# Optimization experiments

Measured on AMD Instinct MI355X. Metric: run time of the kernel, lower is better.

The kernel has to match this reference:

```python
import jax, jax.numpy as jnp
import numpy as np

LEAK = 0.2
NUM_GRAPHS = 64


def _gat(h_in, src, dst, eh, W, att_src, att_dst, att_edge, lin_edge_W, bias, N):
    # PyG GATConv with edge_dim, concat=False (mean over heads)
    H, C = att_src.shape
    h = (h_in @ W).reshape(N, H, C)                      # [N,H,C]
    e = (eh @ lin_edge_W).reshape(-1, H, C)              # [Eaug,H,C]
    a_s = jnp.einsum('nhc,hc->nh', h, att_src)           # [N,H]
    a_d = jnp.einsum('nhc,hc->nh', h, att_dst)
    a_e = jnp.einsum('ehc,hc->eh', e, att_edge)          # [Eaug,H]
    score = jax.nn.leaky_relu(a_s[src] + a_d[dst] + a_e, LEAK)
    # scatter-softmax over incoming edges of each destination node
    m = jax.ops.segment_max(score, dst, num_segments=N)
    ex = jnp.exp(score - m[dst])
    den = jax.ops.segment_sum(ex, dst, num_segments=N)
    alpha = ex / den[dst]                                # [Eaug,H]
    out = jax.ops.segment_sum(alpha[:, :, None] * h[src], dst, num_segments=N)
    return out.mean(axis=1) + bias                       # concat=False -> head mean


def setup_inputs() -> dict:
    key = jax.random.key(0)
    ks = jax.random.split(key, 32)
    N, E, F, FE, HID, H, NT = 30000, 480000, 64, 16, 64, 4, 16
    Cin1 = F + HID
    s = 0.05
    d = {
        'x': jax.random.normal(ks[0], (N, F), jnp.float32),
        'edge_attr': jax.random.normal(ks[1], (E, FE), jnp.float32),
        'node_emb': jax.random.normal(ks[2], (NT, HID), jnp.float32) * s,
        'edge_W': jax.random.normal(ks[3], (FE, HID), jnp.float32) * s,
        'edge_b': jnp.zeros((HID,), jnp.float32),
        'W1': jax.random.normal(ks[4], (Cin1, H * HID), jnp.float32) * s,
        'as1': jax.random.normal(ks[5], (H, HID), jnp.float32) * s,
        'ad1': jax.random.normal(ks[6], (H, HID), jnp.float32) * s,
        'ae1': jax.random.normal(ks[7], (H, HID), jnp.float32) * s,
        'leW1': jax.random.normal(ks[8], (HID, H * HID), jnp.float32) * s,
        'b1': jnp.zeros((HID,), jnp.float32),
        'W2': jax.random.normal(ks[9], (HID, H * HID), jnp.float32) * s,
        'as2': jax.random.normal(ks[10], (H, HID), jnp.float32) * s,
        'ad2': jax.random.normal(ks[11], (H, HID), jnp.float32) * s,
        'ae2': jax.random.normal(ks[12], (H, HID), jnp.float32) * s,
        'leW2': jax.random.normal(ks[13], (HID, H * HID), jnp.float32) * s,
        'b2': jnp.zeros((HID,), jnp.float32),
        'sage_Wl': jax.random.normal(ks[14], (HID, HID), jnp.float32) * s,
        'sage_bl': jnp.zeros((HID,), jnp.float32),
        'sage_Wr': jax.random.normal(ks[15], (HID, HID), jnp.float32) * s,
        'lin1_W': jax.random.normal(ks[16], (HID, HID), jnp.float32) * s,
        'lin1_b': jnp.zeros((HID,), jnp.float32),
        'lin2_W': jax.random.normal(ks[17], (HID, HID), jnp.float32) * s,
        'lin2_b': jnp.zeros((HID,), jnp.float32),
        'tel_W': jax.random.normal(ks[18], (HID, 1), jnp.float32) * s,
        'tel_b': jnp.zeros((1,), jnp.float32),
        'comp_W': jax.random.normal(ks[19], (HID, 1), jnp.float32) * s,
        'comp_b': jnp.zeros((1,), jnp.float32),
        'pch_W': jax.random.normal(ks[20], (HID, 1), jnp.float32) * s,
        'pch_b': jnp.zeros((1,), jnp.float32),
        'edge_index': jax.random.randint(ks[21], (2, E), 0, N, jnp.int32),
        'batch': jnp.sort(jax.random.randint(ks[22], (N,), 0, NUM_GRAPHS, jnp.int32)),
        'node_type': jax.random.randint(ks[23], (N,), 0, NT, jnp.int32),
    }
    return d


def reference(x, edge_attr, node_emb, edge_W, edge_b,
              W1, as1, ad1, ae1, leW1, b1,
              W2, as2, ad2, ae2, leW2, b2,
              sage_Wl, sage_bl, sage_Wr,
              lin1_W, lin1_b, lin2_W, lin2_b,
              tel_W, tel_b, comp_W, comp_b, pch_W, pch_b,
              edge_index, batch, node_type):
    N = x.shape[0]
    src0, dst0 = edge_index[0], edge_index[1]

    h0 = jnp.concatenate([x, node_emb[node_type]], axis=-1)   # [N, F+HID]
    eh = edge_attr @ edge_W + edge_b                          # [E, HID]

    # GATConv default add_self_loops=True, fill_value='mean' on edge_attr
    loop = jnp.arange(N, dtype=src0.dtype)
    src = jnp.concatenate([src0, loop])
    dst = jnp.concatenate([dst0, loop])
    eh_aug = jnp.concatenate([eh, jnp.broadcast_to(eh.mean(axis=0), (N, eh.shape[1]))], axis=0)

    h1 = jax.nn.elu(_gat(h0, src, dst, eh_aug, W1, as1, ad1, ae1, leW1, b1, N))
    h2 = jax.nn.elu(_gat(h1, src, dst, eh_aug, W2, as2, ad2, ae2, leW2, b2, N))

    # SAGEConv: mean neighbor aggregation (src->dst) + root transform
    deg = jax.ops.segment_sum(jnp.ones_like(dst0, dtype=h2.dtype), dst0, num_segments=N)
    agg = jax.ops.segment_sum(h2[src0], dst0, num_segments=N) / jnp.clip(deg, 1.0)[:, None]
    h3 = jax.nn.elu(agg @ sage_Wl + sage_bl + h2 @ sage_Wr)

    # global mean pool per graph
    cnt = jax.ops.segment_sum(jnp.ones((N,), h3.dtype), batch, num_segments=NUM_GRAPHS)
    g = jax.ops.segment_sum(h3, batch, num_segments=NUM_GRAPHS) / jnp.clip(cnt, 1.0)[:, None]

    g = jax.nn.elu(g @ lin1_W + lin1_b)                       # dropout inactive (eval)
    g = g @ lin2_W + lin2_b
    return (g @ tel_W + tel_b, g @ comp_W + comp_b, g @ pch_W + pch_b)
```

## Files before the change

### kernel.cpp

```cpp
#include <hip/hip_runtime.h>
#include <hip/hip_fp16.h>
#include <math.h>

#define NN 30000
#define NE 480000
#define FEA 16
#define HID 64
#define NG 64
#define LEAKK 0.2f

#define S_AEL1   0
#define S_AEL2   4
#define S_KF1    16
#define S_C1     80
#define S_KF2    88
#define S_C2     152
#define S_MS1    160
#define S_MD1    672
#define S_MS2    1184
#define S_MD2    1440
#define S_EAS    1700

#define BT1H 0
#define BT1L 20480
#define BT2H 40960
#define BT2L 57344
#define BT3H 73728
#define BT3L 81920

typedef __attribute__((ext_vector_type(8))) short short8;
typedef __attribute__((ext_vector_type(4))) float f32x4;

__device__ __forceinline__ float eluf(float v) { return v > 0.f ? v : expm1f(v); }
__device__ __forceinline__ float leakyf(float v) { return v >= 0.f ? v : LEAKK * v; }
__device__ __forceinline__ void fma4(float4& a, float w, const float4& x) {
    a.x += w * x.x; a.y += w * x.y; a.z += w * x.z; a.w += w * x.w;
}
__device__ __forceinline__ unsigned bf16pack(float a, float b) {
    unsigned ua = __float_as_uint(a), ub = __float_as_uint(b);
    ua = (ua + 0x7FFFu + ((ua >> 16) & 1u)) >> 16;
    ub = (ub + 0x7FFFu + ((ub >> 16) & 1u)) >> 16;
    return ua | (ub << 16);
}
__device__ __forceinline__ unsigned short bf1(float v) {
    unsigned u = __float_as_uint(v);
    return (unsigned short)((u + 0x7FFFu + ((u >> 16) & 1u)) >> 16);
}
__device__ __forceinline__ float bf1tof(unsigned short h) {
    return __uint_as_float(((unsigned)h) << 16);
}
__device__ __forceinline__ uint2 bfpack4(float a, float b, float c, float d) {
    return make_uint2(bf16pack(a, b), bf16pack(c, d));
}
__device__ __forceinline__ float4 bf16x4(uint2 p) {
    float4 r;
    r.x = __uint_as_float(p.x << 16);
    r.y = __uint_as_float(p.x & 0xFFFF0000u);
    r.z = __uint_as_float(p.y << 16);
    r.w = __uint_as_float(p.y & 0xFFFF0000u);
    return r;
}
__device__ __forceinline__ unsigned h2pack(float a, float b) {
    __half2 h = __floats2half2_rn(a, b);
    return *(unsigned*)&h;
}
__device__ __forceinline__ float2 h2unpack(unsigned u) {
    __half2 h = *(__half2*)&u;
    return __half22float2(h);
}
__device__ __forceinline__ float4 h4tof(uint2 p) {
    float2 lo = h2unpack(p.x), hi = h2unpack(p.y);
    return make_float4(lo.x, lo.y, hi.x, hi.y);
}
__device__ __forceinline__ float4 escore4(float4 a, float4 b, float4 c) {
    float4 r;
    r.x = expf(leakyf(a.x + b.x + c.x));
    r.y = expf(leakyf(a.y + b.y + c.y));
    r.z = expf(leakyf(a.z + b.z + c.z));
    r.w = expf(leakyf(a.w + b.w + c.w));
    return r;
}


__global__ __launch_bounds__(256) void cm_prepw_kernel(
    const int* __restrict__ dst, const float* __restrict__ EA,
    int* __restrict__ cnt, int* __restrict__ rank,
    const float* __restrict__ W1, const float* __restrict__ W2,
    const float* __restrict__ Wl, const float* __restrict__ Wr,
    const float* __restrict__ emb,
    const float* __restrict__ leW1, const float* __restrict__ aew1,
    const float* __restrict__ leW2, const float* __restrict__ aew2,
    const float* __restrict__ edge_W, const float* __restrict__ edge_b,
    const float* __restrict__ as1, const float* __restrict__ ad1,
    const float* __restrict__ as2, const float* __restrict__ ad2,
    const int* __restrict__ batch,
    unsigned short* __restrict__ BT,
    float* __restrict__ S, int* __restrict__ goff) {
    int t = threadIdx.x, bx = blockIdx.x;
    if (bx < 176) {
        int i = bx * 256 + t;
        float v = 0.f;
        int dsti = -1;
        if (i < 16384) {
            int kk = i >> 6, c = i & 63;
            int h = kk >> 6, k = kk & 63;
            v = 0.25f * W1[k * 256 + h * 64 + c];
            dsti = BT1H + c * 320 + kk;
        } else if (i < 20480) {
            int j2 = i - 16384;
            int r2 = j2 >> 6, c = j2 & 63;
            int tau = r2 >> 2, h = r2 & 3;
            float acc = 0.f;
            for (int j = 0; j < 64; j++)
                acc += emb[tau * 64 + j] * W1[(64 + j) * 256 + h * 64 + c];
            v = 0.25f * acc;
            dsti = BT1H + c * 320 + 256 + r2;
        } else if (i < 36864) {
            int j = i - 20480;
            int kk = j >> 6, c = j & 63;
            int h = kk >> 6, k = kk & 63;
            v = 0.25f * W2[k * 256 + h * 64 + c];
            dsti = BT2H + c * 256 + kk;
        } else if (i < 45056) {
            int j = i - 36864;
            int k = j >> 6, c = j & 63;
            v = (k < 64) ? Wl[k * 64 + c] : Wr[(k - 64) * 64 + c];
            dsti = BT3H + c * 128 + k;
        }
        if (dsti >= 0) {
            unsigned short hi = bf1(v);
            unsigned short lo = bf1(v - bf1tof(hi));
            BT[dsti] = hi;
            BT[dsti + 20480 - ((dsti >= BT2H) ? ((dsti >= BT3H) ? 12288 : 4096) : 0)] = lo;
        }
        return;
    }
    if (bx < 178) {
        int i = (bx - 176) * 256 + t;
        int k = i >> 2, h = i & 3;
        float s = 0.f, d = 0.f;
        for (int c = 0; c < 64; c++) {
            float w = W1[k * 256 + h * 64 + c];
            s += w * as1[h * 64 + c];
            d += w * ad1[h * 64 + c];
        }
        S[S_MS1 + i] = s; S[S_MD1 + i] = d;
        return;
    }
    if (bx == 178) {
        int k = t >> 2, h = t & 3;
        float s = 0.f, d = 0.f;
        for (int c = 0; c < 64; c++) {
            float w = W2[k * 256 + h * 64 + c];
            s += w * as2[h * 64 + c];
            d += w * ad2[h * 64 + c];
        }
        S[S_MS2 + t] = s; S[S_MD2 + t] = d;
        return;
    }
    if (bx == 179) {
        __shared__ float M1s[256], M2s[256];
        {
            int k = t >> 2, h = t & 3;
            float m1 = 0.f, m2 = 0.f;
            for (int c = 0; c < 64; c++) {
                m1 += leW1[k * 256 + h * 64 + c] * aew1[h * 64 + c];
                m2 += leW2[k * 256 + h * 64 + c] * aew2[h * 64 + c];
            }
            M1s[t] = m1; M2s[t] = m2;
        }
        __syncthreads();
        if (t < 64) {
            int f = t >> 2, h = t & 3;
            float k1 = 0.f, k2 = 0.f;
            for (int k = 0; k < 64; k++) {
                k1 += edge_W[f * 64 + k] * M1s[k * 4 + h];
                k2 += edge_W[f * 64 + k] * M2s[k * 4 + h];
            }
            S[S_KF1 + t] = k1; S[S_KF2 + t] = k2;
        } else if (t < 68) {
            int h = t - 64;
            float c1 = 0.f, c2 = 0.f;
            for (int k = 0; k < 64; k++) {
                c1 += edge_b[k] * M1s[k * 4 + h];
                c2 += edge_b[k] * M2s[k * 4 + h];
            }
            S[S_C1 + h] = c1; S[S_C2 + h] = c2;
        }
        return;
    }
    if (bx == 180) {
        if (t > NG) return;
        int lo = 0, hi = NN;
        while (lo < hi) {
            int mid = (lo + hi) >> 1;
            if (batch[mid] < t) lo = mid + 1; else hi = mid;
        }
        goff[t] = lo;
        return;
    }
    if (bx < 245) {
        __shared__ float4 red4[16];
        int cb = bx - 181;
        int c4 = (t & 3) * 4;
        int r0 = cb * 64 + (t >> 2);
        float4 a0 = {0, 0, 0, 0}, a1 = a0, a2 = a0, a3 = a0;
        for (int r = r0; r < NE; r += 16384) {
            int r1 = r + 4096, r2 = r + 8192, r3 = r + 12288;
            float4 v0 = *(const float4*)(EA + (size_t)r * FEA + c4);
            float4 v1 = (r1 < NE) ? *(const float4*)(EA + (size_t)r1 * FEA + c4)
                                  : make_float4(0, 0, 0, 0);
            float4 v2 = (r2 < NE) ? *(const float4*)(EA + (size_t)r2 * FEA + c4)
                                  : make_float4(0, 0, 0, 0);
            float4 v3 = (r3 < NE) ? *(const float4*)(EA + (size_t)r3 * FEA + c4)
                                  : make_float4(0, 0, 0, 0);
            a0.x += v0.x; a0.y += v0.y; a0.z += v0.z; a0.w += v0.w;
            a1.x += v1.x; a1.y += v1.y; a1.z += v1.z; a1.w += v1.w;
            a2.x += v2.x; a2.y += v2.y; a2.z += v2.z; a2.w += v2.w;
            a3.x += v3.x; a3.y += v3.y; a3.z += v3.z; a3.w += v3.w;
        }
        float4 acc;
        acc.x = (a0.x + a1.x) + (a2.x + a3.x);
        acc.y = (a0.y + a1.y) + (a2.y + a3.y);
        acc.z = (a0.z + a1.z) + (a2.z + a3.z);
        acc.w = (a0.w + a1.w) + (a2.w + a3.w);
#pragma unroll
        for (int mask = 4; mask < 64; mask <<= 1) {
            acc.x += __shfl_xor(acc.x, mask, 64);
            acc.y += __shfl_xor(acc.y, mask, 64);
            acc.z += __shfl_xor(acc.z, mask, 64);
            acc.w += __shfl_xor(acc.w, mask, 64);
        }
        int lane = t & 63, wid = t >> 6;
        if (lane < 4) red4[wid * 4 + lane] = acc;
        __syncthreads();
        if (t < 4) {
            float4 a = red4[t], b = red4[4 + t], c = red4[8 + t], d = red4[12 + t];
            atomicAdd(&S[S_EAS + t * 4 + 0], a.x + b.x + c.x + d.x);
            atomicAdd(&S[S_EAS + t * 4 + 1], a.y + b.y + c.y + d.y);
            atomicAdd(&S[S_EAS + t * 4 + 2], a.z + b.z + c.z + d.z);
            atomicAdd(&S[S_EAS + t * 4 + 3], a.w + b.w + c.w + d.w);
        }
        return;
    }
    int base = (bx - 245) * 1024;
    int e0 = base + t, e1 = e0 + 256, e2 = e0 + 512, e3 = e0 + 768;
    int d0 = (e0 < NE) ? dst[e0] : 0;
    int d1 = (e1 < NE) ? dst[e1] : 0;
    int d2 = (e2 < NE) ? dst[e2] : 0;
    int d3 = (e3 < NE) ? dst[e3] : 0;
    int r0 = 0, r1 = 0, r2 = 0, r3 = 0;
    if (e0 < NE) r0 = atomicAdd(&cnt[d0 * 8], 1);
    if (e1 < NE) r1 = atomicAdd(&cnt[d1 * 8], 1);
    if (e2 < NE) r2 = atomicAdd(&cnt[d2 * 8], 1);
    if (e3 < NE) r3 = atomicAdd(&cnt[d3 * 8], 1);
    if (e0 < NE) rank[e0] = r0;
    if (e1 < NE) rank[e1] = r1;
    if (e2 < NE) rank[e2] = r2;
    if (e3 < NE) rank[e3] = r3;
}

__global__ void scan_blocks_kernel(const int* __restrict__ cnt, int* __restrict__ eoff,
                                   int* __restrict__ bsum) {
    __shared__ int wsum[16];
    int t = threadIdx.x;
    int i = blockIdx.x * 1024 + t;
    int v = (i < NN) ? cnt[i * 8] : 0;
    int lane = t & 63;
    int incl = v;
#pragma unroll
    for (int ofs = 1; ofs < 64; ofs <<= 1) {
        int u = __shfl_up(incl, ofs, 64);
        if (lane >= ofs) incl += u;
    }
    int wid = t >> 6;
    if (lane == 63) wsum[wid] = incl;
    __syncthreads();
    if (t < 16) {
        int s = wsum[t];
#pragma unroll
        for (int ofs = 1; ofs < 16; ofs <<= 1) {
            int u = __shfl_up(s, ofs, 64);
            if (t >= ofs) s += u;
        }
        wsum[t] = s;
    }
    __syncthreads();
    int excl = incl - v + (wid > 0 ? wsum[wid - 1] : 0);
    if (i < NN) eoff[i] = excl;
    if (t == 1023) bsum[blockIdx.x] = excl + v;
}

__global__ __launch_bounds__(256) void scanadd_attn_kernel(
    const int* __restrict__ bsum, int* __restrict__ eoff,
    const float* __restrict__ x, const float* __restrict__ node_emb,
    const int* __restrict__ node_type, float* __restrict__ S,
    float* __restrict__ as_, float* __restrict__ ad_, unsigned* __restrict__ xb) {
    __shared__ float xt[64 * 132];
    __shared__ float ms[512], md[512];
    __shared__ int ntS[64];
    int t = threadIdx.x;
    if (blockIdx.x < 118) {
        int j = blockIdx.x >> 2;
        int pref = 0;
        for (int u = 0; u < j; u++) pref += bsum[u];
        int i = blockIdx.x * 256 + t;
        if (i < NN) eoff[i] += pref;
        if (i == 0) eoff[NN] = NE;
        return;
    }
    if (blockIdx.x == 118) {
        if (t < 8) {
            int h = t & 3;
            const float* KF = (t < 4) ? (S + S_KF1) : (S + S_KF2);
            const float* C  = (t < 4) ? (S + S_C1)  : (S + S_C2);
            float acc = (float)NE * C[h];
            for (int f = 0; f < 16; f++) acc += S[S_EAS + f] * KF[f * 4 + h];
            S[((t < 4) ? S_AEL1 : S_AEL2) + h] = acc;
        }
        return;
    }
    int n0 = (blockIdx.x - 119) * 64;
    if (t < 64) {
        int n = n0 + t;
        ntS[t] = (n < NN) ? node_type[n] : 0;
    }
    for (int i = t; i < 512; i += 256) { ms[i] = S[S_MS1 + i]; md[i] = S[S_MD1 + i]; }
    __syncthreads();
    for (int i = t; i < 1024; i += 256) {
        int r = i >> 4, c4 = (i & 15) * 4;
        int n = n0 + r;
        float4 f = {0, 0, 0, 0};
        if (n < NN) f = *(const float4*)(x + (size_t)n * 64 + c4);
        *(float4*)&xt[r * 132 + c4] = f;
    }
    for (int i = t; i < 1024; i += 256) {
        int r = i >> 4, c4 = (i & 15) * 4;
        int n = n0 + r;
        float4 f = {0, 0, 0, 0};
        if (n < NN) f = *(const float4*)(node_emb + (size_t)ntS[r] * 64 + c4);
        *(float4*)&xt[r * 132 + 64 + c4] = f;
    }
    __syncthreads();
    for (int i = t; i < 2048; i += 256) {
        int r = i >> 5, u = i & 31;
        int n = n0 + r;
        if (n < NN)
            xb[(size_t)n * 32 + u] = bf16pack(xt[r * 132 + 2 * u], xt[r * 132 + 2 * u + 1]);
    }
    int r = t >> 2, h = t & 3;
    float s = 0.f, d = 0.f;
#pragma unroll 8
    for (int k = 0; k < 128; k++) {
        float xv = xt[r * 132 + k];
        s += xv * ms[k * 4 + h];
        d += xv * md[k * 4 + h];
    }
    int n = n0 + r;
    if (n < NN) { as_[n * 4 + h] = s; ad_[n * 4 + h] = d; }
}

__global__ __launch_bounds__(256) void scatter_proj_kernel(
    const int* __restrict__ src, const int* __restrict__ dst,
    const float* __restrict__ EA, const float* __restrict__ S,
    const float* __restrict__ as_, const float* __restrict__ ad_,
    const int* __restrict__ node_type,
    const int* __restrict__ eoff, const int* __restrict__ rank,
    uint4* __restrict__ recs) {
    __shared__ float KF1s[64], KF2s[64], Cs[8];
    int t = threadIdx.x;
    if (t < 64) { KF1s[t] = S[S_KF1 + t]; KF2s[t] = S[S_KF2 + t]; }
    else if (t < 72) { int q = t - 64; Cs[q] = (q < 4) ? S[S_C1 + q] : S[S_C2 + q - 4]; }
    __syncthreads();
    int e0 = blockIdx.x * 512 + t;
#pragma unroll
    for (int u = 0; u < 2; u++) {
        int e = e0 + u * 256;
        if (e < NE) {
            int s = src[e], d = dst[e];
            float a1[4], a2[4];
#pragma unroll
            for (int h = 0; h < 4; h++) { a1[h] = Cs[h]; a2[h] = Cs[4 + h]; }
            const float4* EA4 = (const float4*)(EA + (size_t)e * FEA);
#pragma unroll
            for (int q = 0; q < 4; q++) {
                float4 v = EA4[q];
                float vv[4] = {v.x, v.y, v.z, v.w};
#pragma unroll
                for (int j = 0; j < 4; j++) {
                    int f = q * 4 + j;
#pragma unroll
                    for (int h = 0; h < 4; h++) {
                        a1[h] += vv[j] * KF1s[f * 4 + h];
                        a2[h] += vv[j] * KF2s[f * 4 + h];
                    }
                }
            }
            int pos = eoff[d] + rank[e];
            float4 asv = ((const float4*)as_)[s];
            float4 adv = ((const float4*)ad_)[d];
            float4 w1 = escore4(asv, adv, make_float4(a1[0], a1[1], a1[2], a1[3]));
            uint4 lo = make_uint4(h2pack(w1.x, w1.y), h2pack(w1.z, w1.w),
                                  h2pack(a2[0], a2[1]), h2pack(a2[2], a2[3]));
            uint4 hi = make_uint4((unsigned)(s | (node_type[s] << 16)), (unsigned)d, 0u, 0u);
            recs[2 * pos] = lo;
            recs[2 * pos + 1] = hi;
        }
    }
}

__global__ __launch_bounds__(256) void score2_kernel(
    uint4* __restrict__ recs,
    const float* __restrict__ as_, const float* __restrict__ ad_,
    int* __restrict__ sepc) {
    int p = blockIdx.x * 256 + threadIdx.x;
    uint2 a2h = ((const uint2*)recs)[4 * p + 1];
    int2 sd = ((const int2*)recs)[4 * p + 2];
    int s = sd.x & 0xFFFF;
    float4 w2 = escore4(((const float4*)as_)[s], ((const float4*)ad_)[sd.y], h4tof(a2h));
    ((uint2*)recs)[4 * p + 1] = make_uint2(h2pack(w2.x, w2.y), h2pack(w2.z, w2.w));
    sepc[p] = sd.x;
}

__global__ __launch_bounds__(256) void agg_gat1_kernel(
    const int* __restrict__ eoff, const uint4* __restrict__ recs,
    const unsigned* __restrict__ xb,
    const int* __restrict__ node_type,
    const float* __restrict__ as_, const float* __restrict__ ad_,
    const float* __restrict__ S, uint2* __restrict__ aggb) {
    int n = blockIdx.x * 4 + (threadIdx.x >> 6);
    if (n >= NN) return;
    int lane = threadIdx.x & 63;
    int sub = lane >> 4, ch = lane & 15;
    const uint2* Xb = (const uint2*)xb;
    const int* RI = (const int*)recs;
    const uint2* RW = (const uint2*)recs;
    float4 asn = ((const float4*)as_)[n];
    float4 adn = ((const float4*)ad_)[n];
    float4 a0 = {0, 0, 0, 0}, a1 = a0, a2 = a0, a3 = a0, dn = a0, tw = a0;
    int b = eoff[n], e_end = eoff[n + 1];
    int nE = e_end - b;
    int i = sub;
    for (; i + 4 < nE; i += 8) {
        int p0 = b + i, p1 = p0 + 4;
        int q0 = RI[8 * p0 + 4], q1 = RI[8 * p1 + 4];
        int s0 = q0 & 0xFFFF, t0 = q0 >> 16;
        int s1 = q1 & 0xFFFF, t1 = q1 >> 16;
        float4 w0 = h4tof(RW[4 * p0]), w1 = h4tof(RW[4 * p1]);
        float4 x0 = bf16x4(Xb[(size_t)s0 * 16 + ch]);
        float4 x1 = bf16x4(Xb[(size_t)s1 * 16 + ch]);
        fma4(a0, w0.x, x0); fma4(a1, w0.y, x0); fma4(a2, w0.z, x0); fma4(a3, w0.w, x0);
        fma4(a0, w1.x, x1); fma4(a1, w1.y, x1); fma4(a2, w1.z, x1); fma4(a3, w1.w, x1);
        dn.x += w0.x + w1.x; dn.y += w0.y + w1.y;
        dn.z += w0.z + w1.z; dn.w += w0.w + w1.w;
        if (ch == t0) { tw.x += w0.x; tw.y += w0.y; tw.z += w0.z; tw.w += w0.w; }
        if (ch == t1) { tw.x += w1.x; tw.y += w1.y; tw.z += w1.z; tw.w += w1.w; }
    }
    for (; i < nE; i += 4) {
        int p0 = b + i;
        int q0 = RI[8 * p0 + 4];
        int s0 = q0 & 0xFFFF, t0 = q0 >> 16;
        float4 w0 = h4tof(RW[4 * p0]);
        float4 x0 = bf16x4(Xb[(size_t)s0 * 16 + ch]);
        fma4(a0, w0.x, x0); fma4(a1, w0.y, x0); fma4(a2, w0.z, x0); fma4(a3, w0.w, x0);
        dn.x += w0.x; dn.y += w0.y; dn.z += w0.z; dn.w += w0.w;
        if (ch == t0) { tw.x += w0.x; tw.y += w0.y; tw.z += w0.z; tw.w += w0.w; }
    }
    if (sub == 0) {
        const float inv = 1.f / (float)NE;
        float e0 = expf(leakyf(asn.x + adn.x + S[S_AEL1 + 0] * inv));
        float e1 = expf(leakyf(asn.y + adn.y + S[S_AEL1 + 1] * inv));
        float e2 = expf(leakyf(asn.z + adn.z + S[S_AEL1 + 2] * inv));
        float e3 = expf(leakyf(asn.w + adn.w + S[S_AEL1 + 3] * inv));
        float4 xs = bf16x4(Xb[(size_t)n * 16 + ch]);
        fma4(a0, e0, xs); fma4(a1, e1, xs); fma4(a2, e2, xs); fma4(a3, e3, xs);
        dn.x += e0; dn.y += e1; dn.z += e2; dn.w += e3;
        int tn = node_type[n];
        if (ch == tn) { tw.x += e0; tw.y += e1; tw.z += e2; tw.w += e3; }
    }
#pragma unroll
    for (int mask = 16; mask < 64; mask <<= 1) {
        a0.x += __shfl_xor(a0.x, mask, 64); a0.y += __shfl_xor(a0.y, mask, 64);
        a0.z += __shfl_xor(a0.z, mask, 64); a0.w += __shfl_xor(a0.w, mask, 64);
        a1.x += __shfl_xor(a1.x, mask, 64); a1.y += __shfl_xor(a1.y, mask, 64);
        a1.z += __shfl_xor(a1.z, mask, 64); a1.w += __shfl_xor(a1.w, mask, 64);
        a2.x += __shfl_xor(a2.x, mask, 64); a2.y += __shfl_xor(a2.y, mask, 64);
        a2.z += __shfl_xor(a2.z, mask, 64); a2.w += __shfl_xor(a2.w, mask, 64);
        a3.x += __shfl_xor(a3.x, mask, 64); a3.y += __shfl_xor(a3.y, mask, 64);
        a3.z += __shfl_xor(a3.z, mask, 64); a3.w += __shfl_xor(a3.w, mask, 64);
        dn.x += __shfl_xor(dn.x, mask, 64); dn.y += __shfl_xor(dn.y, mask, 64);
        dn.z += __shfl_xor(dn.z, mask, 64); dn.w += __shfl_xor(dn.w, mask, 64);
        tw.x += __shfl_xor(tw.x, mask, 64); tw.y += __shfl_xor(tw.y, mask, 64);
        tw.z += __shfl_xor(tw.z, mask, 64); tw.w += __shfl_xor(tw.w, mask, 64);
    }
    if (sub == 0) {
        float i0 = 1.f / dn.x, i1 = 1.f / dn.y, i2 = 1.f / dn.z, i3 = 1.f / dn.w;
        uint2* A2 = aggb + (size_t)n * 80;
        A2[ch]      = bfpack4(a0.x * i0, a0.y * i0, a0.z * i0, a0.w * i0);
        A2[16 + ch] = bfpack4(a1.x * i1, a1.y * i1, a1.z * i1, a1.w * i1);
        A2[32 + ch] = bfpack4(a2.x * i2, a2.y * i2, a2.z * i2, a2.w * i2);
        A2[48 + ch] = bfpack4(a3.x * i3, a3.y * i3, a3.z * i3, a3.w * i3);
        A2[64 + ch] = bfpack4(tw.x * i0, tw.y * i1, tw.z * i2, tw.w * i3);
    }
}

__global__ __launch_bounds__(256) void agg_gat2_kernel(
    const int* __restrict__ eoff, const uint4* __restrict__ recs,
    const unsigned* __restrict__ h1b,
    const float* __restrict__ as_, const float* __restrict__ ad_,
    const float* __restrict__ S, uint2* __restrict__ aggb) {
    int n = blockIdx.x * 4 + (threadIdx.x >> 6);
    if (n >= NN) return;
    int lane = threadIdx.x & 63;
    int sub = lane >> 4, ch = lane & 15;
    const uint2* Xb = (const uint2*)h1b;
    const int* RI = (const int*)recs;
    const uint2* RW = (const uint2*)recs;
    float4 asn = ((const float4*)as_)[n];
    float4 adn = ((const float4*)ad_)[n];
    float4 a0 = {0, 0, 0, 0}, a1 = a0, a2 = a0, a3 = a0, dn = a0;
    int b = eoff[n], e = eoff[n + 1];
    int nE = e - b;
    int i = sub;
    for (; i + 4 < nE; i += 8) {
        int p0 = b + i, p1 = p0 + 4;
        int s0 = RI[8 * p0 + 4] & 0xFFFF, s1 = RI[8 * p1 + 4] & 0xFFFF;
        float4 w0 = h4tof(RW[4 * p0 + 1]), w1 = h4tof(RW[4 * p1 + 1]);
        float4 x0 = bf16x4(Xb[(size_t)s0 * 16 + ch]);
        float4 x1 = bf16x4(Xb[(size_t)s1 * 16 + ch]);
        fma4(a0, w0.x, x0); fma4(a1, w0.y, x0); fma4(a2, w0.z, x0); fma4(a3, w0.w, x0);
        fma4(a0, w1.x, x1); fma4(a1, w1.y, x1); fma4(a2, w1.z, x1); fma4(a3, w1.w, x1);
        dn.x += w0.x + w1.x; dn.y += w0.y + w1.y;
        dn.z += w0.z + w1.z; dn.w += w0.w + w1.w;
    }
    for (; i < nE; i += 4) {
        int p0 = b + i;
        int s0 = RI[8 * p0 + 4] & 0xFFFF;
        float4 w0 = h4tof(RW[4 * p0 + 1]);
        float4 x0 = bf16x4(Xb[(size_t)s0 * 16 + ch]);
        fma4(a0, w0.x, x0); fma4(a1, w0.y, x0); fma4(a2, w0.z, x0); fma4(a3, w0.w, x0);
        dn.x += w0.x; dn.y += w0.y; dn.z += w0.z; dn.w += w0.w;
    }
    if (sub == 0) {
        const float inv = 1.f / (float)NE;
        float e0 = expf(leakyf(asn.x + adn.x + S[S_AEL2 + 0] * inv));
        float e1 = expf(leakyf(asn.y + adn.y + S[S_AEL2 + 1] * inv));
        float e2 = expf(leakyf(asn.z + adn.z + S[S_AEL2 + 2] * inv));
        float e3 = expf(leakyf(asn.w + adn.w + S[S_AEL2 + 3] * inv));
        float4 xs = bf16x4(Xb[(size_t)n * 16 + ch]);
        fma4(a0, e0, xs); fma4(a1, e1, xs); fma4(a2, e2, xs); fma4(a3, e3, xs);
        dn.x += e0; dn.y += e1; dn.z += e2; dn.w += e3;
    }
#pragma unroll
    for (int mask = 16; mask < 64; mask <<= 1) {
        a0.x += __shfl_xor(a0.x, mask, 64); a0.y += __shfl_xor(a0.y, mask, 64);
        a0.z += __shfl_xor(a0.z, mask, 64); a0.w += __shfl_xor(a0.w, mask, 64);
        a1.x += __shfl_xor(a1.x, mask, 64); a1.y += __shfl_xor(a1.y, mask, 64);
        a1.z += __shfl_xor(a1.z, mask, 64); a1.w += __shfl_xor(a1.w, mask, 64);
        a2.x += __shfl_xor(a2.x, mask, 64); a2.y += __shfl_xor(a2.y, mask, 64);
        a2.z += __shfl_xor(a2.z, mask, 64); a2.w += __shfl_xor(a2.w, mask, 64);
        a3.x += __shfl_xor(a3.x, mask, 64); a3.y += __shfl_xor(a3.y, mask, 64);
        a3.z += __shfl_xor(a3.z, mask, 64); a3.w += __shfl_xor(a3.w, mask, 64);
        dn.x += __shfl_xor(dn.x, mask, 64); dn.y += __shfl_xor(dn.y, mask, 64);
        dn.z += __shfl_xor(dn.z, mask, 64); dn.w += __shfl_xor(dn.w, mask, 64);
    }
    if (sub == 0) {
        float i0 = 1.f / dn.x, i1 = 1.f / dn.y, i2 = 1.f / dn.z, i3 = 1.f / dn.w;
        uint2* A2 = aggb + (size_t)n * 64;
        A2[ch]      = bfpack4(a0.x * i0, a0.y * i0, a0.z * i0, a0.w * i0);
        A2[16 + ch] = bfpack4(a1.x * i1, a1.y * i1, a1.z * i1, a1.w * i1);
        A2[32 + ch] = bfpack4(a2.x * i2, a2.y * i2, a2.z * i2, a2.w * i2);
        A2[48 + ch] = bfpack4(a3.x * i3, a3.y * i3, a3.z * i3, a3.w * i3);
    }
}

template <int K, bool DOATT>
__global__ __launch_bounds__(256) void gemm_mfma_kernel(
    const unsigned* __restrict__ A, const unsigned short* __restrict__ bth,
    const unsigned short* __restrict__ btl,
    const float* __restrict__ bias, float* __restrict__ out,
    unsigned short* __restrict__ out16,
    const float* __restrict__ ms_g, const float* __restrict__ md_g,
    float* __restrict__ as_, float* __restrict__ ad_) {
    int t = threadIdx.x;
    int w = t >> 6, l = t & 63;
    int lr = l & 15, lg = l >> 4;
    int m0 = blockIdx.x * 64 + w * 16;
    int am = m0 + lr;
    bool av = am < NN;
    const short8* Arow = (const short8*)A + (size_t)am * (K / 8);
    short8 zz = {0, 0, 0, 0, 0, 0, 0, 0};
    f32x4 acc[4];
#pragma unroll
    for (int ct = 0; ct < 4; ct++) acc[ct] = (f32x4){0.f, 0.f, 0.f, 0.f};
#pragma unroll
    for (int k0 = 0; k0 < K; k0 += 32) {
        short8 a = av ? Arow[(k0 >> 3) + lg] : zz;
#pragma unroll
        for (int ct = 0; ct < 4; ct++) {
            int bo = (ct * 16 + lr) * K + k0 + lg * 8;
            short8 bh = *(const short8*)(bth + bo);
            short8 bl = *(const short8*)(btl + bo);
            acc[ct] = __builtin_amdgcn_mfma_f32_16x16x32_bf16(a, bh, acc[ct], 0, 0, 0);
            acc[ct] = __builtin_amdgcn_mfma_f32_16x16x32_bf16(a, bl, acc[ct], 0, 0, 0);
        }
    }
    f32x4 ps[4], pd[4];
    if (DOATT) {
#pragma unroll
        for (int r = 0; r < 4; r++) {
            ps[r] = (f32x4){0.f, 0.f, 0.f, 0.f};
            pd[r] = (f32x4){0.f, 0.f, 0.f, 0.f};
        }
    }
#pragma unroll
    for (int ct = 0; ct < 4; ct++) {
        int col = ct * 16 + lr;
        float bv = bias[col];
        f32x4 ms4, md4;
        if (DOATT) {
            ms4 = ((const f32x4*)ms_g)[col];
            md4 = ((const f32x4*)md_g)[col];
        }
#pragma unroll
        for (int r = 0; r < 4; r++) {
            int m = m0 + lg * 4 + r;
            float o = eluf(acc[ct][r] + bv);
            if (m < NN) {
                if (out) out[(size_t)m * 64 + col] = o;
                if (out16) out16[(size_t)m * 64 + col] = bf1(o);
            }
            if (DOATT) { ps[r] += o * ms4; pd[r] += o * md4; }
        }
    }
    if (DOATT) {
#pragma unroll
        for (int mk = 1; mk < 16; mk <<= 1)
#pragma unroll
            for (int r = 0; r < 4; r++) {
                ps[r][0] += __shfl_xor(ps[r][0], mk, 64);
                ps[r][1] += __shfl_xor(ps[r][1], mk, 64);
                ps[r][2] += __shfl_xor(ps[r][2], mk, 64);
                ps[r][3] += __shfl_xor(ps[r][3], mk, 64);
                pd[r][0] += __shfl_xor(pd[r][0], mk, 64);
                pd[r][1] += __shfl_xor(pd[r][1], mk, 64);
                pd[r][2] += __shfl_xor(pd[r][2], mk, 64);
                pd[r][3] += __shfl_xor(pd[r][3], mk, 64);
            }
        if (lr == 0) {
#pragma unroll
            for (int r = 0; r < 4; r++) {
                int m = m0 + lg * 4 + r;
                if (m < NN) {
                    *(f32x4*)(as_ + (size_t)m * 4) = ps[r];
                    *(f32x4*)(ad_ + (size_t)m * 4) = pd[r];
                }
            }
        }
    }
}

__global__ __launch_bounds__(256) void sage_agg3_kernel(
    const unsigned* __restrict__ h2b,
    const int* __restrict__ eoff, const int* __restrict__ sepc,
    uint2* __restrict__ AB) {
    int n = blockIdx.x * 16 + (threadIdx.x >> 4);
    if (n >= NN) return;
    int l = threadIdx.x & 15;
    const uint2* Hb = (const uint2*)h2b;
    float ax = 0.f, ay = 0.f, az = 0.f, aw = 0.f;
    int b = eoff[n], e_end = eoff[n + 1];
    int idx = b;
    int stop = b + ((e_end - b) & ~7);
    if (idx < stop) {
        int sreg[8];
#pragma unroll
        for (int u = 0; u < 8; u++) sreg[u] = sepc[idx + u] & 0xFFFF;
        idx += 8;
        while (true) {
            int sn[8];
            bool more = idx < stop;
            if (more) {
#pragma unroll
                for (int u = 0; u < 8; u++) sn[u] = sepc[idx + u] & 0xFFFF;
            }
#pragma unroll
            for (int u = 0; u < 8; u++) {
                float4 v = bf16x4(Hb[(size_t)sreg[u] * 16 + l]);
                ax += v.x; ay += v.y; az += v.z; aw += v.w;
            }
            if (!more) break;
#pragma unroll
            for (int u = 0; u < 8; u++) sreg[u] = sn[u];
            idx += 8;
        }
    }
    for (; idx < e_end; idx++) {
        float4 v0 = bf16x4(Hb[(size_t)(sepc[idx] & 0xFFFF) * 16 + l]);
        ax += v0.x; ay += v0.y; az += v0.z; aw += v0.w;
    }
    float dg = (float)(e_end - b);
    if (dg < 1.f) dg = 1.f;
    float inv = 1.f / dg;
    AB[(size_t)n * 32 + l] = bfpack4(ax * inv, ay * inv, az * inv, aw * inv);
    AB[(size_t)n * 32 + 16 + l] = Hb[(size_t)n * 16 + l];
}

__global__ __launch_bounds__(256) void pool_mlp_kernel(
    const float* __restrict__ h3, const int* __restrict__ goff,
    const float* __restrict__ lin1W, const float* __restrict__ lin1b,
    const float* __restrict__ lin2W, const float* __restrict__ lin2b,
    const float* __restrict__ telW, const float* __restrict__ telb,
    const float* __restrict__ compW, const float* __restrict__ compb,
    const float* __restrict__ pchW, const float* __restrict__ pchb,
    float* __restrict__ out) {
    __shared__ float red[256];
    __shared__ float g[64], G1[64], G2[64];
    int gi = blockIdx.x, t = threadIdx.x;
    int c = t & 63, li = t >> 6;
    int b = goff[gi], e = goff[gi + 1];
    float sum = 0.f;
    for (int r = b + li; r < e; r += 4) sum += h3[(size_t)r * HID + c];
    red[t] = sum;
    __syncthreads();
    if (t < 64) {
        float v = red[t] + red[t + 64] + red[t + 128] + red[t + 192];
        float cntf = (float)(e - b);
        if (cntf < 1.f) cntf = 1.f;
        g[t] = v / cntf;
    }
    __syncthreads();
    {
        float part = 0.f;
#pragma unroll
        for (int k = li * 16; k < li * 16 + 16; k++) part += g[k] * lin1W[k * 64 + c];
        red[t] = part;
        __syncthreads();
        if (t < 64)
            G1[c] = eluf(red[c] + red[c + 64] + red[c + 128] + red[c + 192] + lin1b[c]);
        __syncthreads();
    }
    {
        float part = 0.f;
#pragma unroll
        for (int k = li * 16; k < li * 16 + 16; k++) part += G1[k] * lin2W[k * 64 + c];
        red[t] = part;
        __syncthreads();
        if (t < 64)
            G2[c] = red[c] + red[c + 64] + red[c + 128] + red[c + 192] + lin2b[c];
        __syncthreads();
    }
    if (t < 192) {
        int h = t >> 6, k = t & 63;
        const float* W = (h == 0) ? telW : ((h == 1) ? compW : pchW);
        red[t] = G2[k] * W[k];
    }
    __syncthreads();
    if (t < 3) {
        float acc = 0.f;
        for (int k = 0; k < 64; k++) acc += red[t * 64 + k];
        float bb = (t == 0) ? telb[0] : ((t == 1) ? compb[0] : pchb[0]);
        out[t * 64 + gi] = acc + bb;
    }
}

extern "C" void kernel_launch(void* const* d_in, const int* in_sizes, int n_in,
                              void* d_out, int out_size, void* d_ws, size_t ws_size,
                              hipStream_t stream) {
    const float* x        = (const float*)d_in[0];
    const float* EA       = (const float*)d_in[1];
    const float* node_emb = (const float*)d_in[2];
    const float* edge_W   = (const float*)d_in[3];
    const float* edge_b   = (const float*)d_in[4];
    const float* W1       = (const float*)d_in[5];
    const float* as1      = (const float*)d_in[6];
    const float* ad1      = (const float*)d_in[7];
    const float* ae1      = (const float*)d_in[8];
    const float* leW1     = (const float*)d_in[9];
    const float* b1       = (const float*)d_in[10];
    const float* W2       = (const float*)d_in[11];
    const float* as2      = (const float*)d_in[12];
    const float* ad2      = (const float*)d_in[13];
    const float* ae2      = (const float*)d_in[14];
    const float* leW2     = (const float*)d_in[15];
    const float* b2       = (const float*)d_in[16];
    const float* sage_Wl  = (const float*)d_in[17];
    const float* sage_bl  = (const float*)d_in[18];
    const float* sage_Wr  = (const float*)d_in[19];
    const float* lin1_W   = (const float*)d_in[20];
    const float* lin1_b   = (const float*)d_in[21];
    const float* lin2_W   = (const float*)d_in[22];
    const float* lin2_b   = (const float*)d_in[23];
    const float* tel_W    = (const float*)d_in[24];
    const float* tel_b    = (const float*)d_in[25];
    const float* comp_W   = (const float*)d_in[26];
    const float* comp_b   = (const float*)d_in[27];
    const float* pch_W    = (const float*)d_in[28];
    const float* pch_b    = (const float*)d_in[29];
    const int* edge_index = (const int*)d_in[30];
    const int* batch      = (const int*)d_in[31];
    const int* node_type  = (const int*)d_in[32];
    float* outp = (float*)d_out;

    const int* srcp = edge_index;
    const int* dstp = edge_index + NE;

    float* wf = (float*)d_ws;
    constexpr size_t OFF_H3    = 0;
    constexpr size_t OFF_AGG   = OFF_H3 + (size_t)NN * 64;
    constexpr size_t OFF_REC   = OFF_AGG + (size_t)NN * 512;
    constexpr size_t OFF_AS    = OFF_REC + (size_t)NE * 8;
    constexpr size_t OFF_AD    = OFF_AS + (size_t)NN * 4;
    constexpr size_t OFF_SMALL = OFF_AD + (size_t)NN * 4;
    constexpr size_t OFF_BT    = OFF_SMALL + 4096;
    constexpr size_t OFF_XB    = OFF_BT + 45056;
    constexpr size_t OFF_H1B   = OFF_XB + (size_t)NN * 32;
    constexpr size_t OFF_H2B   = OFF_H1B + (size_t)NN * 32;
    constexpr size_t F_TOTAL   = OFF_H2B + (size_t)NN * 32;

    int* wi   = (int*)(wf + F_TOTAL);
    int* cnt  = wi;
    int* rank = wi + NN * 8;
    int* eoff = rank + NE;
    int* sepc = eoff + (NN + 2);
    int* goff = sepc + NE;
    int* bsum = goff + (NG + 1);

    float* h3    = wf + OFF_H3;
    float* aggb  = wf + OFF_AGG;
    uint4* recs  = (uint4*)(wf + OFF_REC);
    float* as_   = wf + OFF_AS;
    float* ad_   = wf + OFF_AD;
    float* S     = wf + OFF_SMALL;
    unsigned short* BT = (unsigned short*)(wf + OFF_BT);
    unsigned* xb  = (unsigned*)(wf + OFF_XB);
    unsigned short* h1b = (unsigned short*)(wf + OFF_H1B);
    unsigned short* h2b = (unsigned short*)(wf + OFF_H2B);

    hipMemsetAsync(S + S_EAS, 0, 16 * sizeof(float), stream);
    hipMemsetAsync(cnt, 0, NN * 8 * sizeof(int), stream);

    cm_prepw_kernel<<<245 + (NE + 1023) / 1024, 256, 0, stream>>>(
        dstp, EA, cnt, rank, W1, W2, sage_Wl, sage_Wr, node_emb,
        leW1, ae1, leW2, ae2, edge_W, edge_b, as1, ad1, as2, ad2, batch,
        BT, S, goff);

    scan_blocks_kernel<<<(NN + 1023) / 1024, 1024, 0, stream>>>(cnt, eoff, bsum);
    scanadd_attn_kernel<<<119 + (NN + 63) / 64, 256, 0, stream>>>(
        bsum, eoff, x, node_emb, node_type, S, as_, ad_, xb);

    scatter_proj_kernel<<<(NE + 511) / 512, 256, 0, stream>>>(
        srcp, dstp, EA, S, as_, ad_, node_type, eoff, rank, recs);

    agg_gat1_kernel<<<(NN + 3) / 4, 256, 0, stream>>>(
        eoff, recs, xb, node_type, as_, ad_, S, (uint2*)aggb);
    gemm_mfma_kernel<320, true><<<(NN + 63) / 64, 256, 0, stream>>>(
        (const unsigned*)aggb, BT + BT1H, BT + BT1L, b1, nullptr, h1b,
        S + S_MS2, S + S_MD2, as_, ad_);

    score2_kernel<<<NE / 256, 256, 0, stream>>>(recs, as_, ad_, sepc);
    agg_gat2_kernel<<<(NN + 3) / 4, 256, 0, stream>>>(
        eoff, recs, (const unsigned*)h1b, as_, ad_, S, (uint2*)aggb);
    gemm_mfma_kernel<256, false><<<(NN + 63) / 64, 256, 0, stream>>>(
        (const unsigned*)aggb, BT + BT2H, BT + BT2L, b2, nullptr, h2b,
        nullptr, nullptr, nullptr, nullptr);

    sage_agg3_kernel<<<(NN + 15) / 16, 256, 0, stream>>>(
        (const unsigned*)h2b, eoff, sepc, (uint2*)aggb);
    gemm_mfma_kernel<128, false><<<(NN + 63) / 64, 256, 0, stream>>>(
        (const unsigned*)aggb, BT + BT3H, BT + BT3L, sage_bl, h3, nullptr,
        nullptr, nullptr, nullptr, nullptr);

    pool_mlp_kernel<<<NG, 256, 0, stream>>>(h3, goff, lin1_W, lin1_b, lin2_W, lin2_b,
                                            tel_W, tel_b, comp_W, comp_b, pch_W, pch_b, outp);
}
```

Baseline: 366.6 us.

## Move node attention/bf16 pack into prep kernel, recompute W1 attention vectors per block

Moves the per-node attention-logit and bf16 packing work (which does not depend on the scan) from the scanadd kernel into the first prep kernel, so it overlaps with the edge-counting atomics. Each of those blocks now recomputes the W1·att projections itself instead of reading them from a separate prep block. The atomic counting blocks are put first. The scanadd kernel shrinks to just the offset fix-up and the edge-attr constant. The cost is redundant projection work in every attention block (512 outputs times 64 MACs each). The prep kernel also uses a larger shared-memory footprint, about 37KB in every block, which may reduce occupancy for the atomic and weight blocks.

```diff
diff --git a/kernel.cpp b/kernel.cpp
--- a/kernel.cpp
+++ b/kernel.cpp
@@ -15,8 +15,6 @@
 #define S_C1     80
 #define S_KF2    88
 #define S_C2     152
-#define S_MS1    160
-#define S_MD1    672
 #define S_MS2    1184
 #define S_MD2    1440
 #define S_EAS    1700
@@ -27,6 +25,15 @@
 #define BT2L 57344
 #define BT3H 73728
 #define BT3L 81920
+
+#define B_CNT  469
+#define B_BT   645
+#define B_MS2  645
+#define B_KF   646
+#define B_GOFF 647
+#define B_EA0  648
+#define B_ATT0 712
+#define B_TOT  1181
 
 typedef __attribute__((ext_vector_type(8))) short short8;
 typedef __attribute__((ext_vector_type(4))) float f32x4;
@@ -94,11 +101,34 @@
     const float* __restrict__ as1, const float* __restrict__ ad1,
     const float* __restrict__ as2, const float* __restrict__ ad2,
     const int* __restrict__ batch,
-    unsigned short* __restrict__ BT,
-    float* __restrict__ S, int* __restrict__ goff) {
+    const float* __restrict__ x, const float* __restrict__ node_emb,
+    const int* __restrict__ node_type,
+    unsigned short* __restrict__ BT, float* __restrict__ S, int* __restrict__ goff,
+    float* __restrict__ as_, float* __restrict__ ad_, unsigned* __restrict__ xb) {
+    __shared__ float xt[64 * 132];
+    __shared__ float msS[512], mdS[512];
+    __shared__ int ntS[64];
     int t = threadIdx.x, bx = blockIdx.x;
-    if (bx < 176) {
-        int i = bx * 256 + t;
+    if (bx < B_CNT) {
+        int base = bx * 1024;
+        int e0 = base + t, e1 = e0 + 256, e2 = e0 + 512, e3 = e0 + 768;
+        int d0 = (e0 < NE) ? dst[e0] : 0;
+        int d1 = (e1 < NE) ? dst[e1] : 0;
+        int d2 = (e2 < NE) ? dst[e2] : 0;
+        int d3 = (e3 < NE) ? dst[e3] : 0;
+        int r0 = 0, r1 = 0, r2 = 0, r3 = 0;
+        if (e0 < NE) r0 = atomicAdd(&cnt[d0 * 8], 1);
+        if (e1 < NE) r1 = atomicAdd(&cnt[d1 * 8], 1);
+        if (e2 < NE) r2 = atomicAdd(&cnt[d2 * 8], 1);
+        if (e3 < NE) r3 = atomicAdd(&cnt[d3 * 8], 1);
+        if (e0 < NE) rank[e0] = r0;
+        if (e1 < NE) rank[e1] = r1;
+        if (e2 < NE) rank[e2] = r2;
+        if (e3 < NE) rank[e3] = r3;
+        return;
+    }
+    if (bx < B_BT) {
+        int i = (bx - B_CNT) * 256 + t;
         float v = 0.f;
         int dsti = -1;
         if (i < 16384) {
@@ -135,19 +165,7 @@
         }
         return;
     }
-    if (bx < 178) {
-        int i = (bx - 176) * 256 + t;
-        int k = i >> 2, h = i & 3;
-        float s = 0.f, d = 0.f;
-        for (int c = 0; c < 64; c++) {
-            float w = W1[k * 256 + h * 64 + c];
-            s += w * as1[h * 64 + c];
-            d += w * ad1[h * 64 + c];
-        }
-        S[S_MS1 + i] = s; S[S_MD1 + i] = d;
-        return;
-    }
-    if (bx == 178) {
+    if (bx == B_MS2) {
         int k = t >> 2, h = t & 3;
         float s = 0.f, d = 0.f;
         for (int c = 0; c < 64; c++) {
@@ -158,8 +176,9 @@
         S[S_MS2 + t] = s; S[S_MD2 + t] = d;
         return;
     }
-    if (bx == 179) {
-        __shared__ float M1s[256], M2s[256];
+    if (bx == B_KF) {
+        float* M1s = xt;
+        float* M2s = xt + 256;
         {
             int k = t >> 2, h = t & 3;
             float m1 = 0.f, m2 = 0.f;
@@ -189,7 +208,7 @@
         }
         return;
     }
-    if (bx == 180) {
+    if (bx == B_GOFF) {
         if (t > NG) return;
         int lo = 0, hi = NN;
         while (lo < hi) {
@@ -199,9 +218,9 @@
         goff[t] = lo;
         return;
     }
-    if (bx < 245) {
-        __shared__ float4 red4[16];
-        int cb = bx - 181;
+    if (bx < B_ATT0) {
+        float4* red4 = (float4*)xt;
+        int cb = bx - B_EA0;
         int c4 = (t & 3) * 4;
         int r0 = cb * 64 + (t >> 2);
         float4 a0 = {0, 0, 0, 0}, a1 = a0, a2 = a0, a3 = a0;
@@ -243,21 +262,53 @@
         }
         return;
     }
-    int base = (bx - 245) * 1024;
-    int e0 = base + t, e1 = e0 + 256, e2 = e0 + 512, e3 = e0 + 768;
-    int d0 = (e0 < NE) ? dst[e0] : 0;
-    int d1 = (e1 < NE) ? dst[e1] : 0;
-    int d2 = (e2 < NE) ? dst[e2] : 0;
-    int d3 = (e3 < NE) ? dst[e3] : 0;
-    int r0 = 0, r1 = 0, r2 = 0, r3 = 0;
-    if (e0 < NE) r0 = atomicAdd(&cnt[d0 * 8], 1);
-    if (e1 < NE) r1 = atomicAdd(&cnt[d1 * 8], 1);
-    if (e2 < NE) r2 = atomicAdd(&cnt[d2 * 8], 1);
-    if (e3 < NE) r3 = atomicAdd(&cnt[d3 * 8], 1);
-    if (e0 < NE) rank[e0] = r0;
-    if (e1 < NE) rank[e1] = r1;
-    if (e2 < NE) rank[e2] = r2;
-    if (e3 < NE) rank[e3] = r3;
+    int n0 = (bx - B_ATT0) * 64;
+    if (t < 64) {
+        int n = n0 + t;
+        ntS[t] = (n < NN) ? node_type[n] : 0;
+    }
+    for (int i = t; i < 512; i += 256) {
+        int k = i >> 2, h = i & 3;
+        float s = 0.f, d = 0.f;
+        for (int c = 0; c < 64; c++) {
+            float w = W1[k * 256 + h * 64 + c];
+            s += w * as1[h * 64 + c];
+            d += w * ad1[h * 64 + c];
+        }
+        msS[i] = s; mdS[i] = d;
+    }
+    __syncthreads();
+    for (int i = t; i < 1024; i += 256) {
+        int r = i >> 4, c4 = (i & 15) * 4;
+        int n = n0 + r;
+        float4 f = {0, 0, 0, 0};
+        if (n < NN) f = *(const float4*)(x + (size_t)n * 64 + c4);
+        *(float4*)&xt[r * 132 + c4] = f;
+    }
+    for (int i = t; i < 1024; i += 256) {
+        int r = i >> 4, c4 = (i & 15) * 4;
+        int n = n0 + r;
+        float4 f = {0, 0, 0, 0};
+        if (n < NN) f = *(const float4*)(node_emb + (size_t)ntS[r] * 64 + c4);
+        *(float4*)&xt[r * 132 + 64 + c4] = f;
+    }
+    __syncthreads();
+    for (int i = t; i < 2048; i += 256) {
+        int r = i >> 5, u = i & 31;
+        int n = n0 + r;
+        if (n < NN)
+            xb[(size_t)n * 32 + u] = bf16pack(xt[r * 132 + 2 * u], xt[r * 132 + 2 * u + 1]);
+    }
+    int r = t >> 2, h = t & 3;
+    float s = 0.f, d = 0.f;
+#pragma unroll 8
+    for (int k = 0; k < 128; k++) {
+        float xv = xt[r * 132 + k];
+        s += xv * msS[k * 4 + h];
+        d += xv * mdS[k * 4 + h];
+    }
+    int n = n0 + r;
+    if (n < NN) { as_[n * 4 + h] = s; ad_[n * 4 + h] = d; }
 }
 
 __global__ void scan_blocks_kernel(const int* __restrict__ cnt, int* __restrict__ eoff,
@@ -291,14 +342,8 @@
     if (t == 1023) bsum[blockIdx.x] = excl + v;
 }
 
-__global__ __launch_bounds__(256) void scanadd_attn_kernel(
-    const int* __restrict__ bsum, int* __restrict__ eoff,
-    const float* __restrict__ x, const float* __restrict__ node_emb,
-    const int* __restrict__ node_type, float* __restrict__ S,
-    float* __restrict__ as_, float* __restrict__ ad_, unsigned* __restrict__ xb) {
-    __shared__ float xt[64 * 132];
-    __shared__ float ms[512], md[512];
-    __shared__ int ntS[64];
+__global__ __launch_bounds__(256) void scanadd_kernel(
+    const int* __restrict__ bsum, int* __restrict__ eoff, float* __restrict__ S) {
     int t = threadIdx.x;
     if (blockIdx.x < 118) {
         int j = blockIdx.x >> 2;
@@ -309,55 +354,14 @@
         if (i == 0) eoff[NN] = NE;
         return;
     }
-    if (blockIdx.x == 118) {
-        if (t < 8) {
-            int h = t & 3;
-            const float* KF = (t < 4) ? (S + S_KF1) : (S + S_KF2);
-            const float* C  = (t < 4) ? (S + S_C1)  : (S + S_C2);
-            float acc = (float)NE * C[h];
-            for (int f = 0; f < 16; f++) acc += S[S_EAS + f] * KF[f * 4 + h];
-            S[((t < 4) ? S_AEL1 : S_AEL2) + h] = acc;
-        }
-        return;
-    }
-    int n0 = (blockIdx.x - 119) * 64;
-    if (t < 64) {
-        int n = n0 + t;
-        ntS[t] = (n < NN) ? node_type[n] : 0;
-    }
-    for (int i = t; i < 512; i += 256) { ms[i] = S[S_MS1 + i]; md[i] = S[S_MD1 + i]; }
-    __syncthreads();
-    for (int i = t; i < 1024; i += 256) {
-        int r = i >> 4, c4 = (i & 15) * 4;
-        int n = n0 + r;
-        float4 f = {0, 0, 0, 0};
-        if (n < NN) f = *(const float4*)(x + (size_t)n * 64 + c4);
-        *(float4*)&xt[r * 132 + c4] = f;
-    }
-    for (int i = t; i < 1024; i += 256) {
-        int r = i >> 4, c4 = (i & 15) * 4;
-        int n = n0 + r;
-        float4 f = {0, 0, 0, 0};
-        if (n < NN) f = *(const float4*)(node_emb + (size_t)ntS[r] * 64 + c4);
-        *(float4*)&xt[r * 132 + 64 + c4] = f;
-    }
-    __syncthreads();
-    for (int i = t; i < 2048; i += 256) {
-        int r = i >> 5, u = i & 31;
-        int n = n0 + r;
-        if (n < NN)
-            xb[(size_t)n * 32 + u] = bf16pack(xt[r * 132 + 2 * u], xt[r * 132 + 2 * u + 1]);
-    }
-    int r = t >> 2, h = t & 3;
-    float s = 0.f, d = 0.f;
-#pragma unroll 8
-    for (int k = 0; k < 128; k++) {
-        float xv = xt[r * 132 + k];
-        s += xv * ms[k * 4 + h];
-        d += xv * md[k * 4 + h];
-    }
-    int n = n0 + r;
-    if (n < NN) { as_[n * 4 + h] = s; ad_[n * 4 + h] = d; }
+    if (t < 8) {
+        int h = t & 3;
+        const float* KF = (t < 4) ? (S + S_KF1) : (S + S_KF2);
+        const float* C  = (t < 4) ? (S + S_C1)  : (S + S_C2);
+        float acc = (float)NE * C[h];
+        for (int f = 0; f < 16; f++) acc += S[S_EAS + f] * KF[f * 4 + h];
+        S[((t < 4) ? S_AEL1 : S_AEL2) + h] = acc;
+    }
 }
 
 __global__ __launch_bounds__(256) void scatter_proj_kernel(
@@ -840,14 +844,13 @@
     hipMemsetAsync(S + S_EAS, 0, 16 * sizeof(float), stream);
     hipMemsetAsync(cnt, 0, NN * 8 * sizeof(int), stream);
 
-    cm_prepw_kernel<<<245 + (NE + 1023) / 1024, 256, 0, stream>>>(
+    cm_prepw_kernel<<<B_TOT, 256, 0, stream>>>(
         dstp, EA, cnt, rank, W1, W2, sage_Wl, sage_Wr, node_emb,
         leW1, ae1, leW2, ae2, edge_W, edge_b, as1, ad1, as2, ad2, batch,
-        BT, S, goff);
+        x, node_emb, node_type, BT, S, goff, as_, ad_, xb);
 
     scan_blocks_kernel<<<(NN + 1023) / 1024, 1024, 0, stream>>>(cnt, eoff, bsum);
-    scanadd_attn_kernel<<<119 + (NN + 63) / 64, 256, 0, stream>>>(
-        bsum, eoff, x, node_emb, node_type, S, as_, ad_, xb);
+    scanadd_kernel<<<119, 256, 0, stream>>>(bsum, eoff, S);
 
     scatter_proj_kernel<<<(NE + 511) / 512, 256, 0, stream>>>(
         srcp, dstp, EA, S, as_, ad_, node_type, eoff, rank, recs);
```

Measured after the change: 385.4 us. +5.1%, slower.
